# Kernel tuning notes

Hardware: AMD Instinct MI355X
Metric: run time of the kernel (lower is better)

The kernel has to match this reference:

```python
import jax, jax.numpy as jnp
import numpy as np

B, T, D, H, TE = 4, 2048, 1024, 8, 2048
EPS = 1e-5

def _ln(x, w, b):
    m = jnp.mean(x, axis=-1, keepdims=True)
    v = jnp.mean((x - m) ** 2, axis=-1, keepdims=True)
    return (x - m) * jax.lax.rsqrt(v + EPS) * w + b

def setup_inputs() -> dict:
    key = jax.random.key(0)
    ks = jax.random.split(key, 16)
    s = 0.02
    inp = {
        'x': jax.random.normal(ks[0], (B, T, D), jnp.float32),
        'emb': jax.random.normal(ks[1], (B, TE), jnp.float32),
        'src_mask': (jax.random.uniform(ks[2], (B, T, 1)) > 0.2).astype(jnp.float32),
        'num_head': H,
        'ln_w': jnp.ones((D,), jnp.float32),
        'ln_b': jnp.zeros((D,), jnp.float32),
        'Wq': jax.random.normal(ks[3], (D, D), jnp.float32) * s,
        'bq': jnp.zeros((D,), jnp.float32),
        'Wk': jax.random.normal(ks[4], (D, D), jnp.float32) * s,
        'bk': jnp.zeros((D,), jnp.float32),
        'Wv': jax.random.normal(ks[5], (D, D), jnp.float32) * s,
        'bv': jnp.zeros((D,), jnp.float32),
        'W_emb': jax.random.normal(ks[6], (TE, 2 * D), jnp.float32) * s,
        'b_emb': jnp.zeros((2 * D,), jnp.float32),
        'ln2_w': jnp.ones((D,), jnp.float32),
        'ln2_b': jnp.zeros((D,), jnp.float32),
        'W_out': jax.random.normal(ks[7], (D, D), jnp.float32) * s,
        'b_out': jnp.zeros((D,), jnp.float32),
    }
    return inp

def reference(x, emb, src_mask, num_head, ln_w, ln_b, Wq, bq, Wk, bk, Wv, bv,
              W_emb, b_emb, ln2_w, ln2_b, W_out, b_out):
    b, t, d = x.shape
    h = num_head
    dh = d // h
    xn = _ln(x, ln_w, ln_b)
    q = xn @ Wq + bq
    k = xn @ Wk + bk + (1.0 - src_mask) * -1000000.0
    q = jax.nn.softmax(q.reshape(b, t, h, dh), axis=-1)   # feature-map softmax over d_head
    k = jax.nn.softmax(k.reshape(b, t, h, dh), axis=1)    # softmax over time
    v = ((xn @ Wv + bv) * src_mask).reshape(b, t, h, dh)
    att = jnp.einsum('bnhd,bnhl->bhdl', k, v)             # [B,H,dh,dh] KV summary
    y = jnp.einsum('bnhd,bhdl->bnhl', q, att).reshape(b, t, d)
    # StylizationBlock (FiLM), dropout p=0
    emb_out = (jax.nn.silu(emb) @ W_emb + b_emb)[:, None, :]  # [B,1,2D]
    scale, shift = jnp.split(emb_out, 2, axis=2)
    hh = _ln(y, ln2_w, ln2_b) * (1.0 + scale) + shift
    hh = jax.nn.silu(hh) @ W_out + b_out
    return x + hh
```

## Files before the change

kernel.cpp:

```cpp
#include <hip/hip_runtime.h>
#include <hip/hip_bf16.h>

#define B_  4
#define T_  2048
#define D_  1024
#define H_  8
#define DH_ 128
#define TE_ 2048
#define M_  (B_*T_)

using short8 = __attribute__((ext_vector_type(8))) short;
using f32x4  = __attribute__((ext_vector_type(4))) float;

__device__ __forceinline__ ushort f2bf(float f) {
  union { float f; unsigned u; } v; v.f = f;
  unsigned r = (v.u + 0x7fffu + ((v.u >> 16) & 1u)) >> 16;
  return (ushort)r;
}
__device__ __forceinline__ float bf2f(ushort h) {
  union { unsigned u; float f; } v; v.u = ((unsigned)h) << 16;
  return v.f;
}

#define GLOAD_LDS16(g, l) __builtin_amdgcn_global_load_lds( \
    (const __attribute__((address_space(1))) void*)(g), \
    (__attribute__((address_space(3))) void*)(l), 16, 0, 0)

__device__ __forceinline__ void gemm_mainloop(
    const ushort* __restrict__ A, int lda,
    const ushort* __restrict__ Bt, int ldb,
    int K, ushort (*As)[128*32], ushort (*Bs)[128*32], f32x4 acc[4][4])
{
  const int tid  = threadIdx.x;
  const int lane = tid & 63;
  const int wave = tid >> 6;
  const int row  = tid >> 2;
  const int ck   = (tid & 3) * 8;
  const int wm   = (wave & 1) * 64;
  const int wn   = (wave >> 1) * 64;
  const int fr   = lane & 15;
  const int quad = lane >> 4;

  const ushort* ga0 = A  + (size_t)row*lda + ck;
  const ushort* ga1 = A  + (size_t)(row+64)*lda + ck;
  const ushort* gb0 = Bt + (size_t)row*ldb + ck;
  const ushort* gb1 = Bt + (size_t)(row+64)*ldb + ck;
  const int woff = wave*512;

  GLOAD_LDS16(ga0, As[0] + woff);
  GLOAD_LDS16(ga1, As[0] + 2048 + woff);
  GLOAD_LDS16(gb0, Bs[0] + woff);
  GLOAD_LDS16(gb1, Bs[0] + 2048 + woff);

#pragma unroll 1
  for (int k0 = 0; k0 < K; k0 += 64) {
    __syncthreads();
    if (k0 + 32 < K) {
      GLOAD_LDS16(ga0 + k0 + 32, As[1] + woff);
      GLOAD_LDS16(ga1 + k0 + 32, As[1] + 2048 + woff);
      GLOAD_LDS16(gb0 + k0 + 32, Bs[1] + woff);
      GLOAD_LDS16(gb1 + k0 + 32, Bs[1] + 2048 + woff);
    }
    {
      short8 af[4], bw[4];
#pragma unroll
      for (int i = 0; i < 4; ++i) {
        af[i] = *(const short8*)&As[0][(wm + i*16 + fr)*32 + quad*8];
        bw[i] = *(const short8*)&Bs[0][(wn + i*16 + fr)*32 + quad*8];
      }
#pragma unroll
      for (int i = 0; i < 4; ++i)
#pragma unroll
        for (int j = 0; j < 4; ++j)
          acc[i][j] = __builtin_amdgcn_mfma_f32_16x16x32_bf16(af[i], bw[j], acc[i][j], 0, 0, 0);
    }
    __syncthreads();
    if (k0 + 64 < K) {
      GLOAD_LDS16(ga0 + k0 + 64, As[0] + woff);
      GLOAD_LDS16(ga1 + k0 + 64, As[0] + 2048 + woff);
      GLOAD_LDS16(gb0 + k0 + 64, Bs[0] + woff);
      GLOAD_LDS16(gb1 + k0 + 64, Bs[0] + 2048 + woff);
    }
    {
      short8 af[4], bw[4];
#pragma unroll
      for (int i = 0; i < 4; ++i) {
        af[i] = *(const short8*)&As[1][(wm + i*16 + fr)*32 + quad*8];
        bw[i] = *(const short8*)&Bs[1][(wn + i*16 + fr)*32 + quad*8];
      }
#pragma unroll
      for (int i = 0; i < 4; ++i)
#pragma unroll
        for (int j = 0; j < 4; ++j)
          acc[i][j] = __builtin_amdgcn_mfma_f32_16x16x32_bf16(af[i], bw[j], acc[i][j], 0, 0, 0);
    }
  }
}

__global__ __launch_bounds__(256) void gemm_qkv_kernel(
    const ushort* __restrict__ xn, const ushort* __restrict__ Wt,
    const float* __restrict__ bq, const float* __restrict__ bk,
    const float* __restrict__ bv, const float* __restrict__ mask,
    ushort* __restrict__ q, ushort* __restrict__ kT, ushort* __restrict__ vT,
    float* __restrict__ ksum)
{
  __shared__ __align__(16) ushort As[2][128*32], Bs[2][128*32];
  const int m0 = blockIdx.x * 128;
  const int nt = blockIdx.y;
  f32x4 acc[4][4] = {};
  gemm_mainloop(xn + (size_t)m0*D_, D_, Wt + (size_t)nt*128*D_, D_, D_, As, Bs, acc);

  const int tid = threadIdx.x;
  const int lane = tid & 63, wave = tid >> 6;
  const int wm = (wave & 1)*64, wn = (wave >> 1)*64;
  const int fr = lane & 15, quad = lane >> 4;
  const int grp = nt >> 3;
  const int h = nt & 7;
  const int hbase = h*DH_;

  if (grp == 0) {
    float* redm = (float*)As;
    float* reds = (float*)As + 256;
    const int wi = wn >> 6;
    float bb[4];
#pragma unroll
    for (int j = 0; j < 4; ++j) bb[j] = bq[hbase + wn + j*16 + fr];
#pragma unroll
    for (int i = 0; i < 4; ++i)
#pragma unroll
      for (int r = 0; r < 4; ++r) {
        float m = -1e30f;
#pragma unroll
        for (int j = 0; j < 4; ++j) m = fmaxf(m, acc[i][j][r] + bb[j]);
        m = fmaxf(m, __shfl_xor(m, 1, 64));
        m = fmaxf(m, __shfl_xor(m, 2, 64));
        m = fmaxf(m, __shfl_xor(m, 4, 64));
        m = fmaxf(m, __shfl_xor(m, 8, 64));
        if (fr == 0) redm[(wm + i*16 + quad*4 + r)*2 + wi] = m;
      }
    __syncthreads();
#pragma unroll
    for (int i = 0; i < 4; ++i)
#pragma unroll
      for (int r = 0; r < 4; ++r) {
        int R = wm + i*16 + quad*4 + r;
        float gm = fmaxf(redm[R*2], redm[R*2+1]);
        float s = 0.f;
#pragma unroll
        for (int j = 0; j < 4; ++j) {
          float e = __expf(acc[i][j][r] + bb[j] - gm);
          acc[i][j][r] = e; s += e;
        }
        s += __shfl_xor(s, 1, 64);
        s += __shfl_xor(s, 2, 64);
        s += __shfl_xor(s, 4, 64);
        s += __shfl_xor(s, 8, 64);
        if (fr == 0) reds[R*2 + wi] = s;
      }
    __syncthreads();
#pragma unroll
    for (int i = 0; i < 4; ++i)
#pragma unroll
      for (int r = 0; r < 4; ++r) {
        int R = wm + i*16 + quad*4 + r;
        float inv = 1.0f / (reds[R*2] + reds[R*2+1]);
        size_t m = (size_t)(m0 + R);
#pragma unroll
        for (int j = 0; j < 4; ++j)
          q[m*D_ + hbase + wn + j*16 + fr] = f2bf(acc[i][j][r] * inv);
      }
  } else {
    const float* bias = (grp == 1) ? bk : bv;
    ushort* dstT = (grp == 1) ? kT : vT;
    const int b = m0 >> 11;
    const int t_in_b = m0 & (T_-1);
#pragma unroll
    for (int j = 0; j < 4; ++j) {
      int col = wn + j*16 + fr;
      float bb = bias[hbase + col];
      float sj = 0.f;
#pragma unroll
      for (int i = 0; i < 4; ++i) {
        int t0 = t_in_b + wm + i*16 + quad*4;
        ushort4 pk; ushort* pp = (ushort*)&pk;
#pragma unroll
        for (int r = 0; r < 4; ++r) {
          int m = m0 + wm + i*16 + quad*4 + r;
          float v = acc[i][j][r] + bb;
          if (grp == 1) {
            v = __expf(v + (1.0f - mask[m]) * -1000000.0f);
            sj += v;
          } else {
            v *= mask[m];
          }
          pp[r] = f2bf(v);
        }
        *(ushort4*)&dstT[((size_t)(b*H_ + h)*DH_ + col)*T_ + t0] = pk;
      }
      if (grp == 1) {
        sj += __shfl_xor(sj, 16, 64);
        sj += __shfl_xor(sj, 32, 64);
        if (quad == 0) atomicAdd(&ksum[(b*H_ + h)*DH_ + col], sj);
      }
    }
  }
}

__global__ __launch_bounds__(256) void gemm_att_kernel(
    const ushort* __restrict__ kT, const ushort* __restrict__ vT,
    float* __restrict__ P)
{
  __shared__ __align__(16) ushort As[2][128*32], Bs[2][128*32];
  const int bh = blockIdx.x;
  const int s  = blockIdx.y;
  f32x4 acc[4][4] = {};
  gemm_mainloop(kT + (size_t)bh*DH_*T_ + s*256, T_,
                vT + (size_t)bh*DH_*T_ + s*256, T_, 256, As, Bs, acc);
  const int tid = threadIdx.x, lane = tid & 63, wave = tid >> 6;
  const int wm = (wave & 1)*64, wn = (wave >> 1)*64, fr = lane & 15, quad = lane >> 4;
  float* Pb = P + ((size_t)(s*32 + bh))*DH_*DH_;
#pragma unroll
  for (int i = 0; i < 4; ++i)
#pragma unroll
    for (int j = 0; j < 4; ++j) {
      int l = wn + j*16 + fr;
      int d0 = wm + i*16 + quad*4;
      float4 pk = {acc[i][j][0], acc[i][j][1], acc[i][j][2], acc[i][j][3]};
      *(float4*)&Pb[(size_t)l*DH_ + d0] = pk;
    }
}

__global__ __launch_bounds__(256) void att_reduce_kernel(
    const float* __restrict__ P, const float* __restrict__ ksum,
    ushort* __restrict__ attT)
{
  const int e = (blockIdx.x*256 + threadIdx.x) * 4;
  float4 s = {0.f, 0.f, 0.f, 0.f};
#pragma unroll
  for (int k = 0; k < 8; ++k) {
    float4 p = *(const float4*)&P[(size_t)k*32*DH_*DH_ + e];
    s.x += p.x; s.y += p.y; s.z += p.z; s.w += p.w;
  }
  const int bh = e >> 14;
  const int d  = e & 127;
  const float4 ks = *(const float4*)&ksum[bh*DH_ + d];
  ushort4 o; ushort* op = (ushort*)&o;
  op[0] = f2bf(s.x / ks.x); op[1] = f2bf(s.y / ks.y);
  op[2] = f2bf(s.z / ks.z); op[3] = f2bf(s.w / ks.w);
  *(ushort4*)&attT[e] = o;
}

__global__ __launch_bounds__(256) void gemm_y_kernel(
    const ushort* __restrict__ q, const ushort* __restrict__ attT,
    ushort* __restrict__ y)
{
  __shared__ __align__(16) ushort As[2][128*32], Bs[2][128*32];
  const int mt = blockIdx.x;
  const int bh = blockIdx.y;
  const int b = bh >> 3, h = bh & 7;
  const int m0 = b*T_ + mt*128;
  f32x4 acc[4][4] = {};
  gemm_mainloop(q + (size_t)m0*D_ + h*DH_, D_,
                attT + (size_t)bh*DH_*DH_, DH_, DH_, As, Bs, acc);
  const int tid = threadIdx.x, lane = tid & 63, wave = tid >> 6;
  const int wm = (wave & 1)*64, wn = (wave >> 1)*64, fr = lane & 15, quad = lane >> 4;
#pragma unroll
  for (int i = 0; i < 4; ++i)
#pragma unroll
    for (int j = 0; j < 4; ++j) {
      int l = wn + j*16 + fr;
#pragma unroll
      for (int r = 0; r < 4; ++r) {
        int m = m0 + wm + i*16 + quad*4 + r;
        y[(size_t)m*D_ + h*DH_ + l] = f2bf(acc[i][j][r]);
      }
    }
}

__global__ __launch_bounds__(256) void gemm_out_kernel(
    const ushort* __restrict__ act, const ushort* __restrict__ WoutT,
    const float* __restrict__ b_out, const float* __restrict__ x,
    float* __restrict__ out)
{
  __shared__ __align__(16) ushort As[2][128*32], Bs[2][128*32];
  const int m0 = blockIdx.x*128, n0 = blockIdx.y*128;
  f32x4 acc[4][4] = {};
  gemm_mainloop(act + (size_t)m0*D_, D_, WoutT + (size_t)n0*D_, D_, D_, As, Bs, acc);
  const int tid = threadIdx.x, lane = tid & 63, wave = tid >> 6;
  const int wm = (wave & 1)*64, wn = (wave >> 1)*64, fr = lane & 15, quad = lane >> 4;
#pragma unroll
  for (int i = 0; i < 4; ++i)
#pragma unroll
    for (int j = 0; j < 4; ++j) {
      int col = n0 + wn + j*16 + fr;
      float bb = b_out[col];
#pragma unroll
      for (int r = 0; r < 4; ++r) {
        int m = m0 + wm + i*16 + quad*4 + r;
        out[(size_t)m*D_ + col] = acc[i][j][r] + bb + x[(size_t)m*D_ + col];
      }
    }
}

__global__ __launch_bounds__(256) void ln1_kernel(
    const float* __restrict__ x, const float* __restrict__ w,
    const float* __restrict__ bb, ushort* __restrict__ xn)
{
  __shared__ float red[8];
  const int row = blockIdx.x, tid = threadIdx.x;
  const int lane = tid & 63, wave = tid >> 6;
  float4 v = *(const float4*)&x[(size_t)row*D_ + tid*4];
  float s  = v.x + v.y + v.z + v.w;
  float sq = v.x*v.x + v.y*v.y + v.z*v.z + v.w*v.w;
#pragma unroll
  for (int off = 32; off; off >>= 1) { s += __shfl_xor(s, off, 64); sq += __shfl_xor(sq, off, 64); }
  if (lane == 0) { red[wave] = s; red[4+wave] = sq; }
  __syncthreads();
  s  = red[0] + red[1] + red[2] + red[3];
  sq = red[4] + red[5] + red[6] + red[7];
  float mean = s * (1.0f/D_);
  float var  = sq * (1.0f/D_) - mean*mean;
  float rstd = rsqrtf(var + 1e-5f);
  int c = tid*4;
  float vv[4] = {v.x, v.y, v.z, v.w};
  ushort4 o; ushort* op = (ushort*)&o;
#pragma unroll
  for (int i = 0; i < 4; ++i) op[i] = f2bf((vv[i]-mean)*rstd*w[c+i] + bb[c+i]);
  *(ushort4*)&xn[(size_t)row*D_ + c] = o;
}

__global__ __launch_bounds__(256) void ln2_film_kernel(
    const ushort* __restrict__ y, const float* __restrict__ w,
    const float* __restrict__ bb, const float* __restrict__ film,
    const float* __restrict__ b_emb, ushort* __restrict__ act)
{
  __shared__ float red[8];
  const int row = blockIdx.x, tid = threadIdx.x;
  const int lane = tid & 63, wave = tid >> 6;
  const int b = row >> 11;
  ushort4 raw = *(const ushort4*)&y[(size_t)row*D_ + tid*4];
  ushort* u = (ushort*)&raw;
  float v[4];
  float s = 0.f, sq = 0.f;
#pragma unroll
  for (int i = 0; i < 4; ++i) { v[i] = bf2f(u[i]); s += v[i]; sq += v[i]*v[i]; }
#pragma unroll
  for (int off = 32; off; off >>= 1) { s += __shfl_xor(s, off, 64); sq += __shfl_xor(sq, off, 64); }
  if (lane == 0) { red[wave] = s; red[4+wave] = sq; }
  __syncthreads();
  s  = red[0] + red[1] + red[2] + red[3];
  sq = red[4] + red[5] + red[6] + red[7];
  float mean = s * (1.0f/D_);
  float var  = sq * (1.0f/D_) - mean*mean;
  float rstd = rsqrtf(var + 1e-5f);
  int c = tid*4;
  ushort4 o; ushort* op = (ushort*)&o;
#pragma unroll
  for (int i = 0; i < 4; ++i) {
    float yn = (v[i]-mean)*rstd*w[c+i] + bb[c+i];
    float scale = film[b*2048 + c+i]        + b_emb[c+i];
    float shift = film[b*2048 + 1024 + c+i] + b_emb[1024 + c+i];
    float hh = yn*(1.f + scale) + shift;
    op[i] = f2bf(hh / (1.f + __expf(-hh)));
  }
  *(ushort4*)&act[(size_t)row*D_ + c] = o;
}

__global__ __launch_bounds__(256) void film_kernel(
    const float* __restrict__ emb, const float* __restrict__ W_emb,
    float* __restrict__ film)
{
  __shared__ float se[256];
  const int j = blockIdx.x*256 + threadIdx.x;
  const int b = blockIdx.y;
  const int t0 = blockIdx.z*256;
  float e = emb[b*TE_ + t0 + threadIdx.x];
  se[threadIdx.x] = e / (1.f + __expf(-e));
  __syncthreads();
  float acc = 0.f;
  for (int tt = 0; tt < 256; ++tt)
    acc += se[tt] * W_emb[(size_t)(t0+tt)*2048 + j];
  atomicAdd(&film[b*2048 + j], acc);
}

__global__ __launch_bounds__(256) void prep_w_kernel(
    const float* __restrict__ Wq, const float* __restrict__ Wk,
    const float* __restrict__ Wv, const float* __restrict__ Wout,
    ushort* __restrict__ Wqkvt, ushort* __restrict__ WoutT)
{
  __shared__ float tile[32][33];
  const int z = blockIdx.z;
  const float* S = (z == 0) ? Wq : (z == 1) ? Wk : (z == 2) ? Wv : Wout;
  ushort* Dst = (z < 3) ? (Wqkvt + (size_t)z*D_*D_) : WoutT;
  const int n0 = blockIdx.x*32, k0 = blockIdx.y*32;
  const int tx = threadIdx.x & 31, ty = threadIdx.x >> 5;
#pragma unroll
  for (int i = 0; i < 4; ++i)
    tile[ty + i*8][tx] = S[(size_t)(k0 + ty + i*8)*D_ + n0 + tx];
  __syncthreads();
#pragma unroll
  for (int i = 0; i < 4; ++i)
    Dst[(size_t)(n0 + ty + i*8)*D_ + k0 + tx] = f2bf(tile[tx][ty + i*8]);
}

extern "C" void kernel_launch(void* const* d_in, const int* in_sizes, int n_in,
                              void* d_out, int out_size, void* d_ws, size_t ws_size,
                              hipStream_t stream)
{
  const float* x     = (const float*)d_in[0];
  const float* emb   = (const float*)d_in[1];
  const float* mask  = (const float*)d_in[2];
  const float* ln_w  = (const float*)d_in[4];
  const float* ln_b  = (const float*)d_in[5];
  const float* Wq    = (const float*)d_in[6];
  const float* bq    = (const float*)d_in[7];
  const float* Wk    = (const float*)d_in[8];
  const float* bk    = (const float*)d_in[9];
  const float* Wv    = (const float*)d_in[10];
  const float* bv    = (const float*)d_in[11];
  const float* W_emb = (const float*)d_in[12];
  const float* b_emb = (const float*)d_in[13];
  const float* ln2_w = (const float*)d_in[14];
  const float* ln2_b = (const float*)d_in[15];
  const float* Wout  = (const float*)d_in[16];
  const float* b_out = (const float*)d_in[17];
  float* out = (float*)d_out;

  char* ws = (char*)d_ws;
  size_t off = 0;
  auto alloc = [&](size_t bytes) { void* p = ws + off; off += (bytes + 255) & ~size_t(255); return p; };
  ushort* xn    = (ushort*)alloc((size_t)M_*D_*2);
  ushort* q     = (ushort*)alloc((size_t)M_*D_*2);
  ushort* kT    = (ushort*)alloc((size_t)M_*D_*2);
  ushort* vT    = (ushort*)alloc((size_t)M_*D_*2);
  ushort* y     = (ushort*)alloc((size_t)M_*D_*2);
  ushort* Wqkvt = (ushort*)alloc((size_t)3*D_*D_*2);
  ushort* WoutT = (ushort*)alloc((size_t)D_*D_*2);
  ushort* attT  = (ushort*)alloc((size_t)B_*H_*DH_*DH_*2);
  float*  film  = (float*)alloc((size_t)B_*2*D_*4);
  float*  ksum  = (float*)alloc((size_t)B_*H_*DH_*4);
  ushort* act   = xn;
  float*  P     = (float*)y;

  hipMemsetAsync(film, 0, (size_t)(B_*2*D_ + B_*H_*DH_)*4, stream);
  prep_w_kernel<<<dim3(32, 32, 4), 256, 0, stream>>>(Wq, Wk, Wv, Wout, Wqkvt, WoutT);
  film_kernel<<<dim3(8, 4, 8), 256, 0, stream>>>(emb, W_emb, film);
  ln1_kernel<<<M_, 256, 0, stream>>>(x, ln_w, ln_b, xn);
  gemm_qkv_kernel<<<dim3(64, 24), 256, 0, stream>>>(xn, Wqkvt, bq, bk, bv, mask, q, kT, vT, ksum);
  gemm_att_kernel<<<dim3(32, 8), 256, 0, stream>>>(kT, vT, P);
  att_reduce_kernel<<<512, 256, 0, stream>>>(P, ksum, attT);
  gemm_y_kernel<<<dim3(16, 32), 256, 0, stream>>>(q, attT, y);
  ln2_film_kernel<<<M_, 256, 0, stream>>>(y, ln2_w, ln2_b, film, b_emb, act);
  gemm_out_kernel<<<dim3(64, 8), 256, 0, stream>>>(act, WoutT, b_out, x, out);
}
```

Measured before the change: 320.8 us.

## Restructure GEMM mainloop, fuse att reduction into GEMM, batch FiLM over B

The shared GEMM mainloop drops the prefetch double buffering. Each 64-wide k step now issues both 32-wide LDS loads, syncs, then runs all MFMAs, which gives up load/compute overlap in exchange for simpler code. The attention-summary GEMM no longer splits T into 8 partial products reduced by a separate kernel. One block per (b,h) now runs the full T reduction and applies the ksum normalisation in its epilogue, removing a launch and the P round-trip but leaving only 32 blocks. The film kernel loads each W_emb element once and applies it to all 4 batch rows, cutting redundant weight reads.

```diff
diff --git a/kernel.cpp b/kernel.cpp
--- a/kernel.cpp
+++ b/kernel.cpp
@@ -47,53 +47,32 @@
   const ushort* gb1 = Bt + (size_t)(row+64)*ldb + ck;
   const int woff = wave*512;
 
-  GLOAD_LDS16(ga0, As[0] + woff);
-  GLOAD_LDS16(ga1, As[0] + 2048 + woff);
-  GLOAD_LDS16(gb0, Bs[0] + woff);
-  GLOAD_LDS16(gb1, Bs[0] + 2048 + woff);
-
-#pragma unroll 1
   for (int k0 = 0; k0 < K; k0 += 64) {
+    GLOAD_LDS16(ga0 + k0,      As[0] + woff);
+    GLOAD_LDS16(ga1 + k0,      As[0] + 2048 + woff);
+    GLOAD_LDS16(gb0 + k0,      Bs[0] + woff);
+    GLOAD_LDS16(gb1 + k0,      Bs[0] + 2048 + woff);
+    GLOAD_LDS16(ga0 + k0 + 32, As[1] + woff);
+    GLOAD_LDS16(ga1 + k0 + 32, As[1] + 2048 + woff);
+    GLOAD_LDS16(gb0 + k0 + 32, Bs[1] + woff);
+    GLOAD_LDS16(gb1 + k0 + 32, Bs[1] + 2048 + woff);
     __syncthreads();
-    if (k0 + 32 < K) {
-      GLOAD_LDS16(ga0 + k0 + 32, As[1] + woff);
-      GLOAD_LDS16(ga1 + k0 + 32, As[1] + 2048 + woff);
-      GLOAD_LDS16(gb0 + k0 + 32, Bs[1] + woff);
-      GLOAD_LDS16(gb1 + k0 + 32, Bs[1] + 2048 + woff);
-    }
-    {
-      short8 af[4], bw[4];
+    short8 af[2][4], bw[2][4];
+#pragma unroll
+    for (int c = 0; c < 2; ++c)
 #pragma unroll
       for (int i = 0; i < 4; ++i) {
-        af[i] = *(const short8*)&As[0][(wm + i*16 + fr)*32 + quad*8];
-        bw[i] = *(const short8*)&Bs[0][(wn + i*16 + fr)*32 + quad*8];
-      }
+        af[c][i] = *(const short8*)&As[c][(wm + i*16 + fr)*32 + quad*8];
+        bw[c][i] = *(const short8*)&Bs[c][(wn + i*16 + fr)*32 + quad*8];
+      }
+#pragma unroll
+    for (int c = 0; c < 2; ++c)
 #pragma unroll
       for (int i = 0; i < 4; ++i)
 #pragma unroll
         for (int j = 0; j < 4; ++j)
-          acc[i][j] = __builtin_amdgcn_mfma_f32_16x16x32_bf16(af[i], bw[j], acc[i][j], 0, 0, 0);
-    }
+          acc[i][j] = __builtin_amdgcn_mfma_f32_16x16x32_bf16(af[c][i], bw[c][j], acc[i][j], 0, 0, 0);
     __syncthreads();
-    if (k0 + 64 < K) {
-      GLOAD_LDS16(ga0 + k0 + 64, As[0] + woff);
-      GLOAD_LDS16(ga1 + k0 + 64, As[0] + 2048 + woff);
-      GLOAD_LDS16(gb0 + k0 + 64, Bs[0] + woff);
-      GLOAD_LDS16(gb1 + k0 + 64, Bs[0] + 2048 + woff);
-    }
-    {
-      short8 af[4], bw[4];
-#pragma unroll
-      for (int i = 0; i < 4; ++i) {
-        af[i] = *(const short8*)&As[1][(wm + i*16 + fr)*32 + quad*8];
-        bw[i] = *(const short8*)&Bs[1][(wn + i*16 + fr)*32 + quad*8];
-      }
-#pragma unroll
-      for (int i = 0; i < 4; ++i)
-#pragma unroll
-        for (int j = 0; j < 4; ++j)
-          acc[i][j] = __builtin_amdgcn_mfma_f32_16x16x32_bf16(af[i], bw[j], acc[i][j], 0, 0, 0);
-    }
   }
 }
 
@@ -208,46 +187,27 @@
 
 __global__ __launch_bounds__(256) void gemm_att_kernel(
     const ushort* __restrict__ kT, const ushort* __restrict__ vT,
-    float* __restrict__ P)
+    const float* __restrict__ ksum, ushort* __restrict__ attT)
 {
   __shared__ __align__(16) ushort As[2][128*32], Bs[2][128*32];
   const int bh = blockIdx.x;
-  const int s  = blockIdx.y;
   f32x4 acc[4][4] = {};
-  gemm_mainloop(kT + (size_t)bh*DH_*T_ + s*256, T_,
-                vT + (size_t)bh*DH_*T_ + s*256, T_, 256, As, Bs, acc);
+  gemm_mainloop(kT + (size_t)bh*DH_*T_, T_,
+                vT + (size_t)bh*DH_*T_, T_, T_, As, Bs, acc);
   const int tid = threadIdx.x, lane = tid & 63, wave = tid >> 6;
   const int wm = (wave & 1)*64, wn = (wave >> 1)*64, fr = lane & 15, quad = lane >> 4;
-  float* Pb = P + ((size_t)(s*32 + bh))*DH_*DH_;
+  const float* ks = ksum + bh*DH_;
 #pragma unroll
   for (int i = 0; i < 4; ++i)
 #pragma unroll
     for (int j = 0; j < 4; ++j) {
       int l = wn + j*16 + fr;
       int d0 = wm + i*16 + quad*4;
-      float4 pk = {acc[i][j][0], acc[i][j][1], acc[i][j][2], acc[i][j][3]};
-      *(float4*)&Pb[(size_t)l*DH_ + d0] = pk;
+      ushort4 pk; ushort* pp = (ushort*)&pk;
+#pragma unroll
+      for (int r = 0; r < 4; ++r) pp[r] = f2bf(acc[i][j][r] / ks[d0 + r]);
+      *(ushort4*)&attT[((size_t)bh*DH_ + l)*DH_ + d0] = pk;
     }
-}
-
-__global__ __launch_bounds__(256) void att_reduce_kernel(
-    const float* __restrict__ P, const float* __restrict__ ksum,
-    ushort* __restrict__ attT)
-{
-  const int e = (blockIdx.x*256 + threadIdx.x) * 4;
-  float4 s = {0.f, 0.f, 0.f, 0.f};
-#pragma unroll
-  for (int k = 0; k < 8; ++k) {
-    float4 p = *(const float4*)&P[(size_t)k*32*DH_*DH_ + e];
-    s.x += p.x; s.y += p.y; s.z += p.z; s.w += p.w;
-  }
-  const int bh = e >> 14;
-  const int d  = e & 127;
-  const float4 ks = *(const float4*)&ksum[bh*DH_ + d];
-  ushort4 o; ushort* op = (ushort*)&o;
-  op[0] = f2bf(s.x / ks.x); op[1] = f2bf(s.y / ks.y);
-  op[2] = f2bf(s.z / ks.z); op[3] = f2bf(s.w / ks.w);
-  *(ushort4*)&attT[e] = o;
 }
 
 __global__ __launch_bounds__(256) void gemm_y_kernel(
@@ -370,17 +330,25 @@
     const float* __restrict__ emb, const float* __restrict__ W_emb,
     float* __restrict__ film)
 {
-  __shared__ float se[256];
-  const int j = blockIdx.x*256 + threadIdx.x;
-  const int b = blockIdx.y;
-  const int t0 = blockIdx.z*256;
-  float e = emb[b*TE_ + t0 + threadIdx.x];
-  se[threadIdx.x] = e / (1.f + __expf(-e));
+  __shared__ float se[4][64];
+  const int tid = threadIdx.x;
+  const int j  = blockIdx.x*256 + tid;
+  const int t0 = blockIdx.y*64;
+  { int b = tid >> 6, tt = tid & 63;
+    float e = emb[b*TE_ + t0 + tt];
+    se[b][tt] = e / (1.f + __expf(-e)); }
   __syncthreads();
-  float acc = 0.f;
-  for (int tt = 0; tt < 256; ++tt)
-    acc += se[tt] * W_emb[(size_t)(t0+tt)*2048 + j];
-  atomicAdd(&film[b*2048 + j], acc);
+  float a0 = 0.f, a1 = 0.f, a2 = 0.f, a3 = 0.f;
+#pragma unroll 8
+  for (int tt = 0; tt < 64; ++tt) {
+    float wv = W_emb[(size_t)(t0 + tt)*2048 + j];
+    a0 += se[0][tt]*wv; a1 += se[1][tt]*wv;
+    a2 += se[2][tt]*wv; a3 += se[3][tt]*wv;
+  }
+  atomicAdd(&film[0*2048 + j], a0);
+  atomicAdd(&film[1*2048 + j], a1);
+  atomicAdd(&film[2*2048 + j], a2);
+  atomicAdd(&film[3*2048 + j], a3);
 }
 
 __global__ __launch_bounds__(256) void prep_w_kernel(
@@ -440,15 +408,13 @@
   float*  film  = (float*)alloc((size_t)B_*2*D_*4);
   float*  ksum  = (float*)alloc((size_t)B_*H_*DH_*4);
   ushort* act   = xn;
-  float*  P     = (float*)y;
 
   hipMemsetAsync(film, 0, (size_t)(B_*2*D_ + B_*H_*DH_)*4, stream);
   prep_w_kernel<<<dim3(32, 32, 4), 256, 0, stream>>>(Wq, Wk, Wv, Wout, Wqkvt, WoutT);
-  film_kernel<<<dim3(8, 4, 8), 256, 0, stream>>>(emb, W_emb, film);
+  film_kernel<<<dim3(8, 32), 256, 0, stream>>>(emb, W_emb, film);
   ln1_kernel<<<M_, 256, 0, stream>>>(x, ln_w, ln_b, xn);
   gemm_qkv_kernel<<<dim3(64, 24), 256, 0, stream>>>(xn, Wqkvt, bq, bk, bv, mask, q, kT, vT, ksum);
-  gemm_att_kernel<<<dim3(32, 8), 256, 0, stream>>>(kT, vT, P);
-  att_reduce_kernel<<<512, 256, 0, stream>>>(P, ksum, attT);
+  gemm_att_kernel<<<32, 256, 0, stream>>>(kT, vT, ksum, attT);
   gemm_y_kernel<<<dim3(16, 32), 256, 0, stream>>>(q, attT, y);
   ln2_film_kernel<<<M_, 256, 0, stream>>>(y, ln2_w, ln2_b, film, b_emb, act);
   gemm_out_kernel<<<dim3(64, 8), 256, 0, stream>>>(act, WoutT, b_out, x, out);
```

Measured after the change: 309.0 us. 1.04x faster.
